# Kernel tuning notes

Measured on AMD Instinct MI355X. Metric: run time of the kernel, lower is better.

The kernel has to match this reference:

```python
import jax, jax.numpy as jnp
import numpy as np

INPUT_SIZE = 64
HIDDEN = 128


def setup_inputs() -> dict:
    key = jax.random.key(0)
    ks = jax.random.split(key, 10)
    B, T, I, H = 512, 1024, INPUT_SIZE, HIDDEN
    s_ih = 1.0 / np.sqrt(H)
    inp = {
        "x": jax.random.normal(ks[0], (B, T, I), dtype=jnp.float32),
        # PyTorch nn.LSTM params, gate order (i, f, g, o)
        "W_ih": jax.random.uniform(ks[1], (4 * H, I), jnp.float32, -s_ih, s_ih),
        "W_hh": jax.random.uniform(ks[2], (4 * H, H), jnp.float32, -s_ih, s_ih),
        "b_ih": jax.random.uniform(ks[3], (4 * H,), jnp.float32, -s_ih, s_ih),
        "b_hh": jax.random.uniform(ks[4], (4 * H,), jnp.float32, -s_ih, s_ih),
        # fc1: 128 -> 256, fc2: 256 -> 1 (PyTorch Linear init bounds)
        "W1": jax.random.uniform(ks[5], (256, H), jnp.float32, -s_ih, s_ih),
        "b1": jax.random.uniform(ks[6], (256,), jnp.float32, -s_ih, s_ih),
        "W2": jax.random.uniform(ks[7], (1, 256), jnp.float32, -1.0 / 16, 1.0 / 16),
        "b2": jax.random.uniform(ks[8], (1,), jnp.float32, -1.0 / 16, 1.0 / 16),
    }
    return inp


def _lstm_last_hidden(x, W_ih, W_hh, b_ih, b_hh):
    B, T, I = x.shape
    H = W_hh.shape[1]
    # Precompute input projection for all timesteps in one big GEMM: [T, B, 4H]
    x_proj = jnp.einsum("bti,gi->tbg", x, W_ih) + (b_ih + b_hh)

    def step(carry, xp_t):
        h, c = carry
        gates = xp_t + h @ W_hh.T  # [B, 4H]
        i_g, f_g, g_g, o_g = jnp.split(gates, 4, axis=-1)
        i_g = jax.nn.sigmoid(i_g)
        f_g = jax.nn.sigmoid(f_g)
        g_g = jnp.tanh(g_g)
        o_g = jax.nn.sigmoid(o_g)
        c = f_g * c + i_g * g_g
        h = o_g * jnp.tanh(c)
        return (h, c), None

    h0 = jnp.zeros((B, H), dtype=x.dtype)
    c0 = jnp.zeros((B, H), dtype=x.dtype)
    (h_T, _), _ = jax.lax.scan(step, (h0, c0), x_proj)
    return h_T  # [B, H], equals output at last timestep


def reference(x, W_ih, W_hh, b_ih, b_hh, W1, b1, W2, b2):
    h_last = _lstm_last_hidden(x, W_ih, W_hh, b_ih, b_hh)  # x[:, -1, :] of LSTM outputs
    y = h_last @ W1.T + b1   # fc1 (no activation in original)
    y = y @ W2.T + b2        # fc2 -> [B, 1]
    return y
```

## Files before the change

### kernel.cpp

```cpp
#include <hip/hip_runtime.h>


#define T_STEPS 1024
#define ISZ 64
#define HSZ 128
#define ZSZ (ISZ + HSZ)
#define BCHUNK 2
#define NTH 1024
#define CLEN 24
#define NGATE 4

#define DPP_X1 0xB1
#define DPP_X2 0x4E
#define DPP_HM 0x141

template<int CTRL>
__device__ __forceinline__ float dppf(float v) {
    return __int_as_float(__builtin_amdgcn_mov_dpp(__float_as_int(v), CTRL, 0xF, 0xF, true));
}

__global__ __launch_bounds__(NTH, 4)
void lstm_fused_kernel(const float* __restrict__ x,
                       const float* __restrict__ W_ih,
                       const float* __restrict__ W_hh,
                       const float* __restrict__ b_ih,
                       const float* __restrict__ b_hh,
                       const float* __restrict__ W1,
                       const float* __restrict__ b1,
                       const float* __restrict__ W2,
                       const float* __restrict__ b2,
                       float* __restrict__ out)
{
    __shared__ __align__(16) float zbuf[2][BCHUNK][ZSZ];
    __shared__ float red[BCHUNK][4];

    const int tid = threadIdx.x;
    const int b0 = blockIdx.x * BCHUNK;
    const int c  = tid & 7;
    const int j  = tid >> 3;
    const int cls = c & 3;
    const int row = c >> 2;

    const bool alpha = (c & 4) != 0;
    const int  c1r = c ^ (alpha ? 7 : 0);
    const bool beta  = (c1r & 2) != 0;
    const bool gamma = ((c1r ^ (beta ? 2 : 0)) & 1) != 0;
    const bool cls3  = (cls == 3);
    const bool cls13 = (cls & 1) != 0;

    const float kk = (cls == 2) ?  2.0f : -1.0f;
    const float aa = (cls == 2) ?  1.0f :  0.0f;
    const float bb = (cls == 2) ? -2.0f :  1.0f;

    float wt[NGATE][CLEN];
    #pragma unroll
    for (int i = 0; i < NGATE; ++i) {
        const float* rih = W_ih + (size_t)(j + HSZ * i) * ISZ;
        const float* rhh = W_hh + (size_t)(j + HSZ * i) * HSZ;
        #pragma unroll
        for (int k = 0; k < CLEN; ++k) {
            const int col = c * CLEN + k;
            wt[i][k] = (col < ISZ) ? rih[col] : rhh[col - ISZ];
        }
    }
    const int g_own = cls * HSZ + j;
    const float bias = b_ih[g_own] + b_hh[g_own];

    if (tid < BCHUNK * HSZ) zbuf[0][tid >> 7][ISZ + (tid & 127)] = 0.0f;
    if (tid >= 256 && tid < 256 + BCHUNK * ISZ) {
        int l = tid - 256;
        zbuf[0][l >> 6][l & 63] =
            x[((size_t)(b0 + (l >> 6)) * T_STEPS + 0) * ISZ + (l & 63)];
    }
    float cst = 0.0f;
    __syncthreads();

    auto step = [&](const float (*__restrict__ zr)[ZSZ],
                    float (*__restrict__ zw)[ZSZ], int t) {
        float xpre = 0.0f;
        const bool pf = (tid >= 512) && (tid < 640) && (t + 1 < T_STEPS);
        if (pf) {
            int l = tid - 512;
            xpre = x[((size_t)(b0 + (l >> 6)) * T_STEPS + (t + 1)) * ISZ + (l & 63)];
        }

        float a[NGATE][BCHUNK];
        #pragma unroll
        for (int i = 0; i < NGATE; ++i) { a[i][0] = 0.0f; a[i][1] = 0.0f; }
        #pragma unroll
        for (int r = 0; r < BCHUNK; ++r) {
            const float4* zp = reinterpret_cast<const float4*>(zr[r]) + c * (CLEN / 4);
            #pragma unroll
            for (int k = 0; k < CLEN / 4; ++k) {
                float4 u = zp[k];
                #pragma unroll
                for (int i = 0; i < NGATE; ++i) {
                    a[i][r] = fmaf(wt[i][4*k  ], u.x, a[i][r]);
                    a[i][r] = fmaf(wt[i][4*k+1], u.y, a[i][r]);
                    a[i][r] = fmaf(wt[i][4*k+2], u.z, a[i][r]);
                    a[i][r] = fmaf(wt[i][4*k+3], u.w, a[i][r]);
                }
            }
        }

        float A000 = a[0][0], A001 = a[1][0], A010 = a[2][0], A011 = a[3][0];
        float A100 = a[3][1], A101 = a[2][1], A110 = a[1][1], A111 = a[0][1];
        float B00 = (alpha ? A100 : A000) + dppf<DPP_HM>(alpha ? A000 : A100);
        float B01 = (alpha ? A101 : A001) + dppf<DPP_HM>(alpha ? A001 : A101);
        float B10 = (alpha ? A110 : A010) + dppf<DPP_HM>(alpha ? A010 : A110);
        float B11 = (alpha ? A111 : A011) + dppf<DPP_HM>(alpha ? A011 : A111);
        float C0  = (beta ? B10 : B00) + dppf<DPP_X2>(beta ? B00 : B10);
        float C1  = (beta ? B11 : B01) + dppf<DPP_X2>(beta ? B01 : B11);
        float S   = (gamma ? C1 : C0) + dppf<DPP_X1>(gamma ? C0 : C1);
        S += bias;

        float e   = __expf(kk * S);
        float act = fmaf(bb, __builtin_amdgcn_rcpf(e + 1.0f), aa);

        float prt = dppf<DPP_X2>(act);
        float m1  = act * prt;
        float fgv = cls3 ? prt : act;
        float x1v = cls13 ? fgv : m1;
        float rcv = dppf<DPP_X1>(x1v);
        float m1v = cls13 ? rcv : x1v;
        float fgf = cls13 ? x1v : rcv;
        cst = fmaf(fgf, cst, m1v);
        float e2 = __expf(2.0f * cst);
        float th = fmaf(-2.0f, __builtin_amdgcn_rcpf(e2 + 1.0f), 1.0f);
        if (cls3) zw[row][ISZ + j] = act * th;

        if (pf) {
            int l = tid - 512;
            zw[l >> 6][l & 63] = xpre;
        }
        __syncthreads();
    };

    for (int t = 0; t < T_STEPS; t += 2) {
        step(zbuf[0], zbuf[1], t);
        step(zbuf[1], zbuf[0], t + 1);
    }

    if (tid < 512) {
        const int b = tid >> 8;
        const int m = tid & 255;
        const float4* w1r = reinterpret_cast<const float4*>(W1 + (size_t)m * HSZ);
        const float4* hr = reinterpret_cast<const float4*>(zbuf[0][b] + ISZ);
        float acc = 0.0f;
        #pragma unroll
        for (int k = 0; k < HSZ / 4; ++k) {
            float4 w = w1r[k];
            float4 h = hr[k];
            acc = fmaf(w.x, h.x, acc);
            acc = fmaf(w.y, h.y, acc);
            acc = fmaf(w.z, h.z, acc);
            acc = fmaf(w.w, h.w, acc);
        }
        float z = (acc + b1[m]) * W2[m];
        #pragma unroll
        for (int off = 32; off >= 1; off >>= 1)
            z += __shfl_down(z, off, 64);
        if ((tid & 63) == 0) red[b][(tid >> 6) & 3] = z;
    }
    __syncthreads();
    if (tid == 0)   out[b0]     = red[0][0] + red[0][1] + red[0][2] + red[0][3] + b2[0];
    if (tid == 256) out[b0 + 1] = red[1][0] + red[1][1] + red[1][2] + red[1][3] + b2[0];
}

extern "C" void kernel_launch(void* const* d_in, const int* in_sizes, int n_in,
                              void* d_out, int out_size, void* d_ws, size_t ws_size,
                              hipStream_t stream) {
    const float* x    = (const float*)d_in[0];
    const float* W_ih = (const float*)d_in[1];
    const float* W_hh = (const float*)d_in[2];
    const float* b_ih = (const float*)d_in[3];
    const float* b_hh = (const float*)d_in[4];
    const float* W1   = (const float*)d_in[5];
    const float* b1   = (const float*)d_in[6];
    const float* W2   = (const float*)d_in[7];
    const float* b2   = (const float*)d_in[8];
    float* out = (float*)d_out;

    lstm_fused_kernel<<<dim3(512 / BCHUNK), dim3(NTH), 0, stream>>>(
        x, W_ih, W_hh, b_ih, b_hh, W1, b1, W2, b2, out);
}
```

Baseline: 1.441 ms.

## Halve block size by having each thread group compute two hidden units

```diff
diff --git a/kernel.cpp b/kernel.cpp
--- a/kernel.cpp
+++ b/kernel.cpp
@@ -6,9 +6,9 @@
 #define HSZ 128
 #define ZSZ (ISZ + HSZ)
 #define BCHUNK 2
-#define NTH 1024
+#define NTH 512
 #define CLEN 24
-#define NGATE 4
+#define NU 2
 
 #define DPP_X1 0xB1
 #define DPP_X2 0x4E
@@ -19,7 +19,7 @@
     return __int_as_float(__builtin_amdgcn_mov_dpp(__float_as_int(v), CTRL, 0xF, 0xF, true));
 }
 
-__global__ __launch_bounds__(NTH, 4)
+__global__ __launch_bounds__(NTH, 2)
 void lstm_fused_kernel(const float* __restrict__ x,
                        const float* __restrict__ W_ih,
                        const float* __restrict__ W_hh,
@@ -36,8 +36,8 @@
 
     const int tid = threadIdx.x;
     const int b0 = blockIdx.x * BCHUNK;
-    const int c  = tid & 7;
-    const int j  = tid >> 3;
+    const int c   = tid & 7;
+    const int grp = tid >> 3;
     const int cls = c & 3;
     const int row = c >> 2;
 
@@ -52,19 +52,26 @@
     const float aa = (cls == 2) ?  1.0f :  0.0f;
     const float bb = (cls == 2) ? -2.0f :  1.0f;
 
-    float wt[NGATE][CLEN];
+    float wt[NU][4][CLEN];
     #pragma unroll
-    for (int i = 0; i < NGATE; ++i) {
-        const float* rih = W_ih + (size_t)(j + HSZ * i) * ISZ;
-        const float* rhh = W_hh + (size_t)(j + HSZ * i) * HSZ;
-        #pragma unroll
-        for (int k = 0; k < CLEN; ++k) {
-            const int col = c * CLEN + k;
-            wt[i][k] = (col < ISZ) ? rih[col] : rhh[col - ISZ];
-        }
-    }
-    const int g_own = cls * HSZ + j;
-    const float bias = b_ih[g_own] + b_hh[g_own];
+    for (int u = 0; u < NU; ++u)
+        #pragma unroll
+        for (int i = 0; i < 4; ++i) {
+            const int g = i * HSZ + 2 * grp + u;
+            const float* rih = W_ih + (size_t)g * ISZ;
+            const float* rhh = W_hh + (size_t)g * HSZ;
+            #pragma unroll
+            for (int k = 0; k < CLEN; ++k) {
+                const int col = c * CLEN + k;
+                wt[u][i][k] = (col < ISZ) ? rih[col] : rhh[col - ISZ];
+            }
+        }
+    float bias[NU];
+    #pragma unroll
+    for (int u = 0; u < NU; ++u) {
+        const int g_own = cls * HSZ + 2 * grp + u;
+        bias[u] = b_ih[g_own] + b_hh[g_own];
+    }
 
     if (tid < BCHUNK * HSZ) zbuf[0][tid >> 7][ISZ + (tid & 127)] = 0.0f;
     if (tid >= 256 && tid < 256 + BCHUNK * ISZ) {
@@ -72,65 +79,79 @@
         zbuf[0][l >> 6][l & 63] =
             x[((size_t)(b0 + (l >> 6)) * T_STEPS + 0) * ISZ + (l & 63)];
     }
-    float cst = 0.0f;
+    float cst[NU] = {0.f, 0.f};
     __syncthreads();
 
     auto step = [&](const float (*__restrict__ zr)[ZSZ],
                     float (*__restrict__ zw)[ZSZ], int t) {
         float xpre = 0.0f;
-        const bool pf = (tid >= 512) && (tid < 640) && (t + 1 < T_STEPS);
+        const bool pf = (tid >= 256) && (tid < 384) && (t + 1 < T_STEPS);
         if (pf) {
-            int l = tid - 512;
+            int l = tid - 256;
             xpre = x[((size_t)(b0 + (l >> 6)) * T_STEPS + (t + 1)) * ISZ + (l & 63)];
         }
 
-        float a[NGATE][BCHUNK];
-        #pragma unroll
-        for (int i = 0; i < NGATE; ++i) { a[i][0] = 0.0f; a[i][1] = 0.0f; }
+        float a[NU][4][BCHUNK];
+        #pragma unroll
+        for (int u = 0; u < NU; ++u)
+            #pragma unroll
+            for (int i = 0; i < 4; ++i) { a[u][i][0] = 0.0f; a[u][i][1] = 0.0f; }
         #pragma unroll
         for (int r = 0; r < BCHUNK; ++r) {
             const float4* zp = reinterpret_cast<const float4*>(zr[r]) + c * (CLEN / 4);
             #pragma unroll
             for (int k = 0; k < CLEN / 4; ++k) {
-                float4 u = zp[k];
+                float4 U = zp[k];
                 #pragma unroll
-                for (int i = 0; i < NGATE; ++i) {
-                    a[i][r] = fmaf(wt[i][4*k  ], u.x, a[i][r]);
-                    a[i][r] = fmaf(wt[i][4*k+1], u.y, a[i][r]);
-                    a[i][r] = fmaf(wt[i][4*k+2], u.z, a[i][r]);
-                    a[i][r] = fmaf(wt[i][4*k+3], u.w, a[i][r]);
-                }
+                for (int u = 0; u < NU; ++u)
+                    #pragma unroll
+                    for (int i = 0; i < 4; ++i) {
+                        a[u][i][r] = fmaf(wt[u][i][4*k  ], U.x, a[u][i][r]);
+                        a[u][i][r] = fmaf(wt[u][i][4*k+1], U.y, a[u][i][r]);
+                        a[u][i][r] = fmaf(wt[u][i][4*k+2], U.z, a[u][i][r]);
+                        a[u][i][r] = fmaf(wt[u][i][4*k+3], U.w, a[u][i][r]);
+                    }
             }
         }
 
-        float A000 = a[0][0], A001 = a[1][0], A010 = a[2][0], A011 = a[3][0];
-        float A100 = a[3][1], A101 = a[2][1], A110 = a[1][1], A111 = a[0][1];
-        float B00 = (alpha ? A100 : A000) + dppf<DPP_HM>(alpha ? A000 : A100);
-        float B01 = (alpha ? A101 : A001) + dppf<DPP_HM>(alpha ? A001 : A101);
-        float B10 = (alpha ? A110 : A010) + dppf<DPP_HM>(alpha ? A010 : A110);
-        float B11 = (alpha ? A111 : A011) + dppf<DPP_HM>(alpha ? A011 : A111);
-        float C0  = (beta ? B10 : B00) + dppf<DPP_X2>(beta ? B00 : B10);
-        float C1  = (beta ? B11 : B01) + dppf<DPP_X2>(beta ? B01 : B11);
-        float S   = (gamma ? C1 : C0) + dppf<DPP_X1>(gamma ? C0 : C1);
-        S += bias;
-
-        float e   = __expf(kk * S);
-        float act = fmaf(bb, __builtin_amdgcn_rcpf(e + 1.0f), aa);
-
-        float prt = dppf<DPP_X2>(act);
-        float m1  = act * prt;
-        float fgv = cls3 ? prt : act;
-        float x1v = cls13 ? fgv : m1;
-        float rcv = dppf<DPP_X1>(x1v);
-        float m1v = cls13 ? rcv : x1v;
-        float fgf = cls13 ? x1v : rcv;
-        cst = fmaf(fgf, cst, m1v);
-        float e2 = __expf(2.0f * cst);
-        float th = fmaf(-2.0f, __builtin_amdgcn_rcpf(e2 + 1.0f), 1.0f);
-        if (cls3) zw[row][ISZ + j] = act * th;
+        float S[NU];
+        #pragma unroll
+        for (int u = 0; u < NU; ++u) {
+            float A000 = a[u][0][0], A001 = a[u][1][0], A010 = a[u][2][0], A011 = a[u][3][0];
+            float A100 = a[u][3][1], A101 = a[u][2][1], A110 = a[u][1][1], A111 = a[u][0][1];
+            float B00 = (alpha ? A100 : A000) + dppf<DPP_HM>(alpha ? A000 : A100);
+            float B01 = (alpha ? A101 : A001) + dppf<DPP_HM>(alpha ? A001 : A101);
+            float B10 = (alpha ? A110 : A010) + dppf<DPP_HM>(alpha ? A010 : A110);
+            float B11 = (alpha ? A111 : A011) + dppf<DPP_HM>(alpha ? A011 : A111);
+            float C0  = (beta ? B10 : B00) + dppf<DPP_X2>(beta ? B00 : B10);
+            float C1  = (beta ? B11 : B01) + dppf<DPP_X2>(beta ? B01 : B11);
+            S[u] = (gamma ? C1 : C0) + dppf<DPP_X1>(gamma ? C0 : C1) + bias[u];
+        }
+
+        float hv[NU];
+        #pragma unroll
+        for (int u = 0; u < NU; ++u) {
+            float e   = __expf(kk * S[u]);
+            float act = fmaf(bb, __builtin_amdgcn_rcpf(e + 1.0f), aa);
+            float prt = dppf<DPP_X2>(act);
+            float m1  = act * prt;
+            float fgv = cls3 ? prt : act;
+            float x1v = cls13 ? fgv : m1;
+            float rcv = dppf<DPP_X1>(x1v);
+            float m1v = cls13 ? rcv : x1v;
+            float fgf = cls13 ? x1v : rcv;
+            cst[u] = fmaf(fgf, cst[u], m1v);
+            float e2 = __expf(2.0f * cst[u]);
+            float th = fmaf(-2.0f, __builtin_amdgcn_rcpf(e2 + 1.0f), 1.0f);
+            hv[u] = act * th;
+        }
+        if (cls3) {
+            float2 hw = { hv[0], hv[1] };
+            *reinterpret_cast<float2*>(&zw[row][ISZ + 2 * grp]) = hw;
+        }
 
         if (pf) {
-            int l = tid - 512;
+            int l = tid - 256;
             zw[l >> 6][l & 63] = xpre;
         }
         __syncthreads();
@@ -141,7 +162,7 @@
         step(zbuf[1], zbuf[0], t + 1);
     }
 
-    if (tid < 512) {
+    {
         const int b = tid >> 8;
         const int m = tid & 255;
         const float4* w1r = reinterpret_cast<const float4*>(W1 + (size_t)m * HSZ);
```

Measured after the change: 1.419 ms. No clear change (-1.5%).
